# Optimization experiments

Measured on AMD Instinct MI355X. Metric: run time of the kernel, lower is better.

Reference implementation:

```python
import jax, jax.numpy as jnp
import numpy as np

BN_EPS = 1e-5


def setup_inputs() -> dict:
    key = jax.random.key(0)
    ks = jax.random.split(key, 5)
    B, N, M, C = 2, 8192, 8192, 3
    return {
        "x": jax.random.normal(ks[0], (B, N, C), dtype=jnp.float32),
        "y": jax.random.normal(ks[1], (B, M, C), dtype=jnp.float32),
        "W1": jax.random.normal(ks[2], (256, 20), dtype=jnp.float32) * 0.1,
        "gamma1": jnp.ones((256,), jnp.float32),
        "beta1": jnp.zeros((256,), jnp.float32),
        "mean1": jnp.zeros((256,), jnp.float32),
        "var1": jnp.ones((256,), jnp.float32),
        "W2": jax.random.normal(ks[3], (128, 256), dtype=jnp.float32) * 0.1,
        "gamma2": jnp.ones((128,), jnp.float32),
        "beta2": jnp.zeros((128,), jnp.float32),
        "mean2": jnp.zeros((128,), jnp.float32),
        "var2": jnp.ones((128,), jnp.float32),
        "W3": jax.random.normal(ks[4], (1, 128), dtype=jnp.float32) * 0.1,
        "k": 20,
    }


def _bn(x, gamma, beta, mean, var):
    # x: [B, C, N]; inference-mode BatchNorm1d
    inv = gamma * jax.lax.rsqrt(var + BN_EPS)
    return x * inv[None, :, None] + (beta - mean * inv)[None, :, None]


def reference(x, y, W1, gamma1, beta1, mean1, var1,
              W2, gamma2, beta2, mean2, var2, W3, k):
    # x: [B,N,C], y: [B,M,C]
    xx = jnp.sum(x * x, axis=-1)                      # [B,N]
    yy = jnp.sum(y * y, axis=-1)                      # [B,M]
    inner = jnp.einsum('bnc,bmc->bnm', x, y)          # [B,N,M]
    # negative squared pairwise distance (as in torch code)
    pd = 2.0 * inner - xx[:, :, None] - yy[:, None, :]
    dist, _ = jax.lax.top_k(pd, k)                    # [B,N,k], descending = k nearest
    feat = jnp.transpose(dist, (0, 2, 1))             # [B,k,N]
    h = jax.nn.relu(_bn(jnp.einsum('oc,bcn->bon', W1, feat), gamma1, beta1, mean1, var1))
    h = jax.nn.relu(_bn(jnp.einsum('oc,bcn->bon', W2, h), gamma2, beta2, mean2, var2))
    out = jax.nn.sigmoid(jnp.einsum('oc,bcn->bon', W3, h))  # [B,1,N]
    return jnp.transpose(out, (0, 2, 1))              # [B,N,1]
```

## Files before the change

kernel.cpp:

```cpp
#include <hip/hip_runtime.h>
#include <hip/hip_bf16.h>
#include <math.h>


#define M_CAND 8192
#define NROWS 16384
#define KSEL 20
#define MPL 8

__device__ __forceinline__ float med3f(float a, float b, float c) {
    return __builtin_amdgcn_fmed3f(a, b, c);
}

__global__ __launch_bounds__(256) void k_prep_y(const float* __restrict__ y,
                                                float4* __restrict__ ys4) {
    int idx = blockIdx.x * 256 + threadIdx.x;
    float y0 = y[idx * 3 + 0];
    float y1 = y[idx * 3 + 1];
    float y2 = y[idx * 3 + 2];
    ys4[idx] = make_float4(y0, y1, y2, y0 * y0 + y1 * y1 + y2 * y2);
}

__global__ __launch_bounds__(256) void k_transpose_w2(const float* __restrict__ w2,
                                                      float* __restrict__ w2t) {
    int idx = blockIdx.x * 256 + threadIdx.x;
    int o = idx >> 8;
    int k = idx & 255;
    w2t[k * 128 + o] = w2[idx];
}

__global__ __launch_bounds__(256, 4) void k_knn(const float* __restrict__ x,
                                                const float4* __restrict__ ys4,
                                                float* __restrict__ dfeat) {
    __shared__ float sm[4][64 * 21];
    const int wid  = threadIdx.x >> 6;
    const int lane = threadIdx.x & 63;
    const int row  = blockIdx.x * 4 + wid;
    const int b    = row >> 13;
    const float x0 = x[row * 3 + 0];
    const float x1 = x[row * 3 + 1];
    const float x2 = x[row * 3 + 2];
    const float tx0 = 2.0f * x0, tx1 = 2.0f * x1, tx2 = 2.0f * x2;
    const float xxn = -(x0 * x0 + x1 * x1 + x2 * x2);
    const float4* yb = ys4 + b * M_CAND;

    float bl[MPL];
#pragma unroll
    for (int j = 0; j < MPL; ++j) bl[j] = -3.0e38f;

    for (int t = 0; t < M_CAND / 256; ++t) {
        const float4* p = yb + t * 256 + lane;
        float4 cc[4];
        cc[0] = p[0]; cc[1] = p[64]; cc[2] = p[128]; cc[3] = p[192];
#pragma unroll
        for (int j = 0; j < 4; ++j) {
            float v = fmaf(tx0, cc[j].x, fmaf(tx1, cc[j].y, fmaf(tx2, cc[j].z, xxn))) - cc[j].w;
#pragma unroll
            for (int jj = MPL - 1; jj >= 1; --jj) bl[jj] = med3f(v, bl[jj - 1], bl[jj]);
            bl[0] = fmaxf(bl[0], v);
        }
    }

    float* myp = sm[wid] + lane * (MPL + 1);
#pragma unroll
    for (int j = 0; j < MPL; ++j) myp[j] = bl[j];
    myp[MPL] = -3.0e38f;
    asm volatile("s_waitcnt lgkmcnt(0)" ::: "memory");

    int ptr = 0;
    float sel = 0.0f;
    for (int r = 0; r < KSEL; ++r) {
        float head = myp[ptr];
        float mx = head;
#pragma unroll
        for (int off = 32; off >= 1; off >>= 1) mx = fmaxf(mx, __shfl_xor(mx, off, 64));
        unsigned long long ball = __ballot(head == mx);
        int winner = (int)__ffsll(ball) - 1;
        ptr += (lane == winner) ? 1 : 0;
        if (lane == r) sel = mx;
    }

    bool need_exact = (__ballot(ptr >= MPL) != 0ULL);
    if (need_exact) {
        float a[KSEL];
#pragma unroll
        for (int j = 0; j < KSEL; ++j) a[j] = -3.0e38f;
        for (int t = 0; t < M_CAND / 256; ++t) {
            const float4* p = yb + t * 256 + lane;
            float4 cc[4];
            cc[0] = p[0]; cc[1] = p[64]; cc[2] = p[128]; cc[3] = p[192];
#pragma unroll
            for (int j = 0; j < 4; ++j) {
                float v = fmaf(tx0, cc[j].x, fmaf(tx1, cc[j].y, fmaf(tx2, cc[j].z, xxn))) - cc[j].w;
#pragma unroll
                for (int jj = KSEL - 1; jj >= 1; --jj) a[jj] = med3f(v, a[jj - 1], a[jj]);
                a[0] = fmaxf(a[0], v);
            }
        }
        float* mq = sm[wid] + lane * (KSEL + 1);
#pragma unroll
        for (int j = 0; j < KSEL; ++j) mq[j] = a[j];
        mq[KSEL] = -3.0e38f;
        asm volatile("s_waitcnt lgkmcnt(0)" ::: "memory");
        int ptr2 = 0;
        for (int r = 0; r < KSEL; ++r) {
            float head = mq[ptr2];
            float mx = head;
#pragma unroll
            for (int off = 32; off >= 1; off >>= 1) mx = fmaxf(mx, __shfl_xor(mx, off, 64));
            unsigned long long ball = __ballot(head == mx);
            int winner = (int)__ffsll(ball) - 1;
            ptr2 += (lane == winner) ? 1 : 0;
            if (lane == r) sel = mx;
        }
    }

    if (lane < KSEL) dfeat[row * KSEL + lane] = sel;
}

__global__ __launch_bounds__(256) void k_mlp1(const float* __restrict__ dfeat,
                                              const float* __restrict__ W1,
                                              const float* __restrict__ g1,
                                              const float* __restrict__ be1,
                                              const float* __restrict__ mu1,
                                              const float* __restrict__ va1,
                                              float* __restrict__ h1g) {
    const int o = threadIdx.x;
    const int rowbase = blockIdx.x * 64;
    float w[KSEL];
#pragma unroll
    for (int j = 0; j < KSEL; j += 4) {
        float4 q = *(const float4*)(W1 + o * KSEL + j);
        w[j] = q.x; w[j + 1] = q.y; w[j + 2] = q.z; w[j + 3] = q.w;
    }
    const float s  = g1[o] * rsqrtf(va1[o] + 1e-5f);
    const float bc = be1[o] - mu1[o] * s;
    for (int r = 0; r < 64; ++r) {
        const float* dr = dfeat + (size_t)(rowbase + r) * KSEL;
        float dv[KSEL];
#pragma unroll
        for (int j = 0; j < KSEL; j += 4) {
            float4 q = *(const float4*)(dr + j);
            dv[j] = q.x; dv[j + 1] = q.y; dv[j + 2] = q.z; dv[j + 3] = q.w;
        }
        float acc0 = 0.f, acc1 = 0.f;
#pragma unroll
        for (int j = 0; j < KSEL; j += 2) {
            acc0 = fmaf(w[j], dv[j], acc0);
            acc1 = fmaf(w[j + 1], dv[j + 1], acc1);
        }
        float hv = fmaxf(0.f, fmaf(s, acc0 + acc1, bc));
        h1g[(size_t)(rowbase + r) * 256 + o] = hv;
    }
}

__global__ __launch_bounds__(256) void k_mlp2(const float* __restrict__ h1g,
                                              const float* __restrict__ W2T,
                                              const float* __restrict__ g2,
                                              const float* __restrict__ be2,
                                              const float* __restrict__ mu2,
                                              const float* __restrict__ va2,
                                              const float* __restrict__ W3,
                                              float* __restrict__ partial) {
    __shared__ float w2l[256 * 64];
    const int t = threadIdx.x;
    const int ohalf = blockIdx.x & 1;
    const int rowbase = (blockIdx.x >> 1) * 64;
    const int obase = ohalf * 64;

    {
        const int oo4 = (t & 15) * 4;
        const int k0  = t >> 4;
        for (int i = 0; i < 16; ++i) {
            int k = k0 + 16 * i;
            float4 q = *(const float4*)(W2T + k * 128 + obase + oo4);
            *(float4*)(&w2l[k * 64 + oo4]) = q;
        }
    }
    __syncthreads();

    const int og = t & 15;
    const int rq = t >> 4;
    float acc[4][4];
#pragma unroll
    for (int r = 0; r < 4; ++r)
#pragma unroll
        for (int i = 0; i < 4; ++i) acc[r][i] = 0.f;

    const float* hrow = h1g + (size_t)(rowbase + rq * 4) * 256;
    for (int kq = 0; kq < 64; ++kq) {
        const int k = kq * 4;
        float4 hq[4];
        hq[0] = *(const float4*)(hrow + 0 * 256 + k);
        hq[1] = *(const float4*)(hrow + 1 * 256 + k);
        hq[2] = *(const float4*)(hrow + 2 * 256 + k);
        hq[3] = *(const float4*)(hrow + 3 * 256 + k);
        float4 wq[4];
        wq[0] = *(const float4*)(&w2l[(k + 0) * 64 + og * 4]);
        wq[1] = *(const float4*)(&w2l[(k + 1) * 64 + og * 4]);
        wq[2] = *(const float4*)(&w2l[(k + 2) * 64 + og * 4]);
        wq[3] = *(const float4*)(&w2l[(k + 3) * 64 + og * 4]);
#pragma unroll
        for (int r = 0; r < 4; ++r) {
            const float* hh = (const float*)&hq[r];
#pragma unroll
            for (int kk = 0; kk < 4; ++kk) {
                const float* ww = (const float*)&wq[kk];
                const float hval = hh[kk];
#pragma unroll
                for (int i = 0; i < 4; ++i)
                    acc[r][i] = fmaf(hval, ww[i], acc[r][i]);
            }
        }
    }

    float s2v[4], b2v[4], w3v[4];
#pragma unroll
    for (int i = 0; i < 4; ++i) {
        const int o = obase + og * 4 + i;
        const float sv = g2[o] * rsqrtf(va2[o] + 1e-5f);
        s2v[i] = sv;
        b2v[i] = be2[o] - mu2[o] * sv;
        w3v[i] = W3[o];
    }
#pragma unroll
    for (int r = 0; r < 4; ++r) {
        float c = 0.f;
#pragma unroll
        for (int i = 0; i < 4; ++i) {
            float h2 = fmaxf(0.f, fmaf(s2v[i], acc[r][i], b2v[i]));
            c = fmaf(w3v[i], h2, c);
        }
#pragma unroll
        for (int off = 8; off >= 1; off >>= 1) c += __shfl_xor(c, off, 64);
        if (og == 0) partial[ohalf * NROWS + rowbase + rq * 4 + r] = c;
    }
}

__global__ __launch_bounds__(256) void k_out(const float* __restrict__ partial,
                                             float* __restrict__ out) {
    int i = blockIdx.x * 256 + threadIdx.x;
    float z = partial[i] + partial[NROWS + i];
    out[i] = 1.0f / (1.0f + expf(-z));
}

extern "C" void kernel_launch(void* const* d_in, const int* in_sizes, int n_in,
                              void* d_out, int out_size, void* d_ws, size_t ws_size,
                              hipStream_t stream) {
    const float* x   = (const float*)d_in[0];
    const float* y   = (const float*)d_in[1];
    const float* W1  = (const float*)d_in[2];
    const float* g1  = (const float*)d_in[3];
    const float* be1 = (const float*)d_in[4];
    const float* mu1 = (const float*)d_in[5];
    const float* va1 = (const float*)d_in[6];
    const float* W2  = (const float*)d_in[7];
    const float* g2  = (const float*)d_in[8];
    const float* be2 = (const float*)d_in[9];
    const float* mu2 = (const float*)d_in[10];
    const float* va2 = (const float*)d_in[11];
    const float* W3  = (const float*)d_in[12];
    float* out = (float*)d_out;

    char* ws = (char*)d_ws;
    float4* ys4  = (float4*)(ws);
    float* dfeat = (float*)(ws + 262144);
    float* w2t   = (float*)(ws + 262144 + 1310720);
    float* h1    = (float*)(ws + 262144 + 1310720 + 131072);
    float* part  = (float*)(ws + 262144 + 1310720 + 131072 + 16777216);

    k_prep_y      <<<64, 256, 0, stream>>>(y, ys4);
    k_transpose_w2<<<128, 256, 0, stream>>>(W2, w2t);
    k_knn         <<<4096, 256, 0, stream>>>(x, ys4, dfeat);
    k_mlp1        <<<256, 256, 0, stream>>>(dfeat, W1, g1, be1, mu1, va1, h1);
    k_mlp2        <<<512, 256, 0, stream>>>(h1, w2t, g2, be2, mu2, va2, W3, part);
    k_out         <<<64, 256, 0, stream>>>(part, out);
}
```

Baseline: 117.2 us.

## Pack candidate pairs for packed-FMA distance, shrink per-lane list, merge prep kernels

Candidate points are repacked so two candidates share float4 slots, and the distance is computed with packed two-wide FMA. The per-lane top list drops from 8 to 4 entries, which cuts med3 work per candidate, but the exact 20-wide fallback pass will trigger more often. The y-prep and W2-transpose kernels are merged into a single launch. mlp1 now uses more blocks with fewer rows each, giving more parallelism.

```diff
diff --git a/kernel.cpp b/kernel.cpp
--- a/kernel.cpp
+++ b/kernel.cpp
@@ -6,31 +6,46 @@
 #define M_CAND 8192
 #define NROWS 16384
 #define KSEL 20
-#define MPL 8
+#define MPL 4
+
+typedef float v2f __attribute__((ext_vector_type(2)));
 
 __device__ __forceinline__ float med3f(float a, float b, float c) {
     return __builtin_amdgcn_fmed3f(a, b, c);
 }
 
-__global__ __launch_bounds__(256) void k_prep_y(const float* __restrict__ y,
-                                                float4* __restrict__ ys4) {
+__device__ __forceinline__ v2f fma2(v2f a, v2f b, v2f c) {
+#if __has_builtin(__builtin_elementwise_fma)
+    return __builtin_elementwise_fma(a, b, c);
+#else
+    v2f r; r.x = fmaf(a.x, b.x, c.x); r.y = fmaf(a.y, b.y, c.y); return r;
+#endif
+}
+
+__global__ __launch_bounds__(256) void k_prep(const float* __restrict__ y,
+                                              const float* __restrict__ w2,
+                                              float4* __restrict__ ysp,
+                                              float* __restrict__ w2t) {
     int idx = blockIdx.x * 256 + threadIdx.x;
-    float y0 = y[idx * 3 + 0];
-    float y1 = y[idx * 3 + 1];
-    float y2 = y[idx * 3 + 2];
-    ys4[idx] = make_float4(y0, y1, y2, y0 * y0 + y1 * y1 + y2 * y2);
-}
-
-__global__ __launch_bounds__(256) void k_transpose_w2(const float* __restrict__ w2,
-                                                      float* __restrict__ w2t) {
-    int idx = blockIdx.x * 256 + threadIdx.x;
-    int o = idx >> 8;
-    int k = idx & 255;
-    w2t[k * 128 + o] = w2[idx];
+    if (idx < 8192) {
+        int b = idx >> 12, q = idx & 4095;
+        const float* p0 = y + (size_t)(b * M_CAND + 2 * q) * 3;
+        float a0 = p0[0], a1 = p0[1], a2 = p0[2];
+        float b0 = p0[3], b1 = p0[4], b2 = p0[5];
+        float nwa = -(a0 * a0 + a1 * a1 + a2 * a2);
+        float nwb = -(b0 * b0 + b1 * b1 + b2 * b2);
+        float4* base = ysp + b * 8192;
+        base[q]        = make_float4(a0, b0, a1, b1);
+        base[4096 + q] = make_float4(a2, b2, nwa, nwb);
+    } else {
+        int j = idx - 8192;
+        int o = j >> 8, kk = j & 255;
+        w2t[kk * 128 + o] = w2[j];
+    }
 }
 
 __global__ __launch_bounds__(256, 4) void k_knn(const float* __restrict__ x,
-                                                const float4* __restrict__ ys4,
+                                                const float4* __restrict__ ysp,
                                                 float* __restrict__ dfeat) {
     __shared__ float sm[4][64 * 21];
     const int wid  = threadIdx.x >> 6;
@@ -40,24 +55,38 @@
     const float x0 = x[row * 3 + 0];
     const float x1 = x[row * 3 + 1];
     const float x2 = x[row * 3 + 2];
-    const float tx0 = 2.0f * x0, tx1 = 2.0f * x1, tx2 = 2.0f * x2;
+    const v2f tx0p = {2.0f * x0, 2.0f * x0};
+    const v2f tx1p = {2.0f * x1, 2.0f * x1};
+    const v2f tx2p = {2.0f * x2, 2.0f * x2};
     const float xxn = -(x0 * x0 + x1 * x1 + x2 * x2);
-    const float4* yb = ys4 + b * M_CAND;
+    const v2f xxnp = {xxn, xxn};
+    const float4* yb = ysp + b * 8192;
 
     float bl[MPL];
 #pragma unroll
     for (int j = 0; j < MPL; ++j) bl[j] = -3.0e38f;
 
-    for (int t = 0; t < M_CAND / 256; ++t) {
-        const float4* p = yb + t * 256 + lane;
-        float4 cc[4];
-        cc[0] = p[0]; cc[1] = p[64]; cc[2] = p[128]; cc[3] = p[192];
-#pragma unroll
-        for (int j = 0; j < 4; ++j) {
-            float v = fmaf(tx0, cc[j].x, fmaf(tx1, cc[j].y, fmaf(tx2, cc[j].z, xxn))) - cc[j].w;
-#pragma unroll
-            for (int jj = MPL - 1; jj >= 1; --jj) bl[jj] = med3f(v, bl[jj - 1], bl[jj]);
-            bl[0] = fmaxf(bl[0], v);
+#pragma unroll 2
+    for (int t = 0; t < 16; ++t) {
+        const float4* pa = yb + t * 256 + lane;
+        const float4* pb = pa + 4096;
+        float4 A[4], Bv[4];
+        A[0]  = pa[0];  A[1]  = pa[64];  A[2]  = pa[128];  A[3]  = pa[192];
+        Bv[0] = pb[0];  Bv[1] = pb[64];  Bv[2] = pb[128];  Bv[3] = pb[192];
+#pragma unroll
+        for (int i = 0; i < 4; ++i) {
+            v2f y0p = {A[i].x,  A[i].y};
+            v2f y1p = {A[i].z,  A[i].w};
+            v2f y2p = {Bv[i].x, Bv[i].y};
+            v2f nwp = {Bv[i].z, Bv[i].w};
+            v2f pd = fma2(tx0p, y0p, fma2(tx1p, y1p, fma2(tx2p, y2p, xxnp))) + nwp;
+            float va = pd.x, vb = pd.y;
+#pragma unroll
+            for (int jj = MPL - 1; jj >= 1; --jj) bl[jj] = med3f(va, bl[jj - 1], bl[jj]);
+            bl[0] = fmaxf(bl[0], va);
+#pragma unroll
+            for (int jj = MPL - 1; jj >= 1; --jj) bl[jj] = med3f(vb, bl[jj - 1], bl[jj]);
+            bl[0] = fmaxf(bl[0], vb);
         }
     }
 
@@ -85,16 +114,26 @@
         float a[KSEL];
 #pragma unroll
         for (int j = 0; j < KSEL; ++j) a[j] = -3.0e38f;
-        for (int t = 0; t < M_CAND / 256; ++t) {
-            const float4* p = yb + t * 256 + lane;
-            float4 cc[4];
-            cc[0] = p[0]; cc[1] = p[64]; cc[2] = p[128]; cc[3] = p[192];
-#pragma unroll
-            for (int j = 0; j < 4; ++j) {
-                float v = fmaf(tx0, cc[j].x, fmaf(tx1, cc[j].y, fmaf(tx2, cc[j].z, xxn))) - cc[j].w;
-#pragma unroll
-                for (int jj = KSEL - 1; jj >= 1; --jj) a[jj] = med3f(v, a[jj - 1], a[jj]);
-                a[0] = fmaxf(a[0], v);
+        for (int t = 0; t < 16; ++t) {
+            const float4* pa = yb + t * 256 + lane;
+            const float4* pb = pa + 4096;
+            float4 A[4], Bv[4];
+            A[0]  = pa[0];  A[1]  = pa[64];  A[2]  = pa[128];  A[3]  = pa[192];
+            Bv[0] = pb[0];  Bv[1] = pb[64];  Bv[2] = pb[128];  Bv[3] = pb[192];
+#pragma unroll
+            for (int i = 0; i < 4; ++i) {
+                v2f y0p = {A[i].x,  A[i].y};
+                v2f y1p = {A[i].z,  A[i].w};
+                v2f y2p = {Bv[i].x, Bv[i].y};
+                v2f nwp = {Bv[i].z, Bv[i].w};
+                v2f pd = fma2(tx0p, y0p, fma2(tx1p, y1p, fma2(tx2p, y2p, xxnp))) + nwp;
+                float va = pd.x, vb = pd.y;
+#pragma unroll
+                for (int jj = KSEL - 1; jj >= 1; --jj) a[jj] = med3f(va, a[jj - 1], a[jj]);
+                a[0] = fmaxf(a[0], va);
+#pragma unroll
+                for (int jj = KSEL - 1; jj >= 1; --jj) a[jj] = med3f(vb, a[jj - 1], a[jj]);
+                a[0] = fmaxf(a[0], vb);
             }
         }
         float* mq = sm[wid] + lane * (KSEL + 1);
@@ -126,7 +165,7 @@
                                               const float* __restrict__ va1,
                                               float* __restrict__ h1g) {
     const int o = threadIdx.x;
-    const int rowbase = blockIdx.x * 64;
+    const int rowbase = blockIdx.x * 16;
     float w[KSEL];
 #pragma unroll
     for (int j = 0; j < KSEL; j += 4) {
@@ -135,7 +174,8 @@
     }
     const float s  = g1[o] * rsqrtf(va1[o] + 1e-5f);
     const float bc = be1[o] - mu1[o] * s;
-    for (int r = 0; r < 64; ++r) {
+#pragma unroll 4
+    for (int r = 0; r < 16; ++r) {
         const float* dr = dfeat + (size_t)(rowbase + r) * KSEL;
         float dv[KSEL];
 #pragma unroll
@@ -263,16 +303,15 @@
     float* out = (float*)d_out;
 
     char* ws = (char*)d_ws;
-    float4* ys4  = (float4*)(ws);
+    float4* ysp  = (float4*)(ws);
     float* dfeat = (float*)(ws + 262144);
     float* w2t   = (float*)(ws + 262144 + 1310720);
     float* h1    = (float*)(ws + 262144 + 1310720 + 131072);
     float* part  = (float*)(ws + 262144 + 1310720 + 131072 + 16777216);
 
-    k_prep_y      <<<64, 256, 0, stream>>>(y, ys4);
-    k_transpose_w2<<<128, 256, 0, stream>>>(W2, w2t);
-    k_knn         <<<4096, 256, 0, stream>>>(x, ys4, dfeat);
-    k_mlp1        <<<256, 256, 0, stream>>>(dfeat, W1, g1, be1, mu1, va1, h1);
-    k_mlp2        <<<512, 256, 0, stream>>>(h1, w2t, g2, be2, mu2, va2, W3, part);
-    k_out         <<<64, 256, 0, stream>>>(part, out);
-}
+    k_prep <<<160, 256, 0, stream>>>(y, W2, ysp, w2t);
+    k_knn  <<<4096, 256, 0, stream>>>(x, ysp, dfeat);
+    k_mlp1 <<<1024, 256, 0, stream>>>(dfeat, W1, g1, be1, mu1, va1, h1);
+    k_mlp2 <<<512, 256, 0, stream>>>(h1, w2t, g2, be2, mu2, va2, W3, part);
+    k_out  <<<64, 256, 0, stream>>>(part, out);
+}
```

Result: slower. 126.3 us (+7.8%).

## Fuse MLP stages, merge prep kernels, shrink per-lane kNN list, SoA candidate layout

Applied to the files above, without the earlier changes.

Merges the y-prep and W2-transpose kernels into one launch. It fuses MLP layer 1, layer 2, the W3 reduction and the sigmoid into a single kernel that keeps h1 in shared memory, so the 16 MB h1 round trip through global memory and two launches go away. The kNN candidates move to a structure-of-arrays layout with the squared norm pre-negated, and the next tile is software-prefetched. The per-lane partial top-k list shrinks from 8 to 4 entries, which cuts med3 work but makes the exact fallback pass more likely to run.

```diff
diff --git a/kernel.cpp b/kernel.cpp
--- a/kernel.cpp
+++ b/kernel.cpp
@@ -6,31 +6,35 @@
 #define M_CAND 8192
 #define NROWS 16384
 #define KSEL 20
-#define MPL 8
+#define MPL 4
 
 __device__ __forceinline__ float med3f(float a, float b, float c) {
     return __builtin_amdgcn_fmed3f(a, b, c);
 }
 
-__global__ __launch_bounds__(256) void k_prep_y(const float* __restrict__ y,
-                                                float4* __restrict__ ys4) {
+__global__ __launch_bounds__(256) void k_prep(const float* __restrict__ y,
+                                              const float* __restrict__ w2,
+                                              float* __restrict__ ys,
+                                              float* __restrict__ w2t) {
     int idx = blockIdx.x * 256 + threadIdx.x;
-    float y0 = y[idx * 3 + 0];
-    float y1 = y[idx * 3 + 1];
-    float y2 = y[idx * 3 + 2];
-    ys4[idx] = make_float4(y0, y1, y2, y0 * y0 + y1 * y1 + y2 * y2);
-}
-
-__global__ __launch_bounds__(256) void k_transpose_w2(const float* __restrict__ w2,
-                                                      float* __restrict__ w2t) {
-    int idx = blockIdx.x * 256 + threadIdx.x;
-    int o = idx >> 8;
-    int k = idx & 255;
-    w2t[k * 128 + o] = w2[idx];
+    if (idx < NROWS) {
+        int b = idx >> 13, m = idx & 8191;
+        const float* p = y + (size_t)idx * 3;
+        float y0 = p[0], y1 = p[1], y2 = p[2];
+        float* base = ys + (size_t)b * 4 * M_CAND + m;
+        base[0]          = y0;
+        base[M_CAND]     = y1;
+        base[2 * M_CAND] = y2;
+        base[3 * M_CAND] = -(y0 * y0 + y1 * y1 + y2 * y2);
+    } else {
+        int j = idx - NROWS;
+        int o = j >> 8, kk = j & 255;
+        w2t[kk * 128 + o] = w2[j];
+    }
 }
 
 __global__ __launch_bounds__(256, 4) void k_knn(const float* __restrict__ x,
-                                                const float4* __restrict__ ys4,
+                                                const float* __restrict__ ys,
                                                 float* __restrict__ dfeat) {
     __shared__ float sm[4][64 * 21];
     const int wid  = threadIdx.x >> 6;
@@ -42,23 +46,33 @@
     const float x2 = x[row * 3 + 2];
     const float tx0 = 2.0f * x0, tx1 = 2.0f * x1, tx2 = 2.0f * x2;
     const float xxn = -(x0 * x0 + x1 * x1 + x2 * x2);
-    const float4* yb = ys4 + b * M_CAND;
+    const float4* q0 = (const float4*)(ys + (size_t)(b * 4 + 0) * M_CAND) + lane;
+    const float4* q1 = (const float4*)(ys + (size_t)(b * 4 + 1) * M_CAND) + lane;
+    const float4* q2 = (const float4*)(ys + (size_t)(b * 4 + 2) * M_CAND) + lane;
+    const float4* q3 = (const float4*)(ys + (size_t)(b * 4 + 3) * M_CAND) + lane;
 
     float bl[MPL];
 #pragma unroll
     for (int j = 0; j < MPL; ++j) bl[j] = -3.0e38f;
 
-    for (int t = 0; t < M_CAND / 256; ++t) {
-        const float4* p = yb + t * 256 + lane;
-        float4 cc[4];
-        cc[0] = p[0]; cc[1] = p[64]; cc[2] = p[128]; cc[3] = p[192];
+    float4 c0 = q0[0], c1 = q1[0], c2 = q2[0], c3 = q3[0];
+#pragma unroll 1
+    for (int t = 0; t < 32; ++t) {
+        const int nt = ((t + 1) & 31) * 64;
+        float4 n0 = q0[nt], n1 = q1[nt], n2 = q2[nt], n3 = q3[nt];
+        const float* e0 = (const float*)&c0;
+        const float* e1 = (const float*)&c1;
+        const float* e2 = (const float*)&c2;
+        const float* e3 = (const float*)&c3;
 #pragma unroll
         for (int j = 0; j < 4; ++j) {
-            float v = fmaf(tx0, cc[j].x, fmaf(tx1, cc[j].y, fmaf(tx2, cc[j].z, xxn))) - cc[j].w;
-#pragma unroll
-            for (int jj = MPL - 1; jj >= 1; --jj) bl[jj] = med3f(v, bl[jj - 1], bl[jj]);
+            float v = fmaf(tx0, e0[j], fmaf(tx1, e1[j], fmaf(tx2, e2[j], xxn))) + e3[j];
+            bl[3] = med3f(v, bl[2], bl[3]);
+            bl[2] = med3f(v, bl[1], bl[2]);
+            bl[1] = med3f(v, bl[0], bl[1]);
             bl[0] = fmaxf(bl[0], v);
         }
+        c0 = n0; c1 = n1; c2 = n2; c3 = n3;
     }
 
     float* myp = sm[wid] + lane * (MPL + 1);
@@ -85,13 +99,15 @@
         float a[KSEL];
 #pragma unroll
         for (int j = 0; j < KSEL; ++j) a[j] = -3.0e38f;
-        for (int t = 0; t < M_CAND / 256; ++t) {
-            const float4* p = yb + t * 256 + lane;
-            float4 cc[4];
-            cc[0] = p[0]; cc[1] = p[64]; cc[2] = p[128]; cc[3] = p[192];
+        for (int t = 0; t < 32; ++t) {
+            float4 d0 = q0[t * 64], d1 = q1[t * 64], d2 = q2[t * 64], d3 = q3[t * 64];
+            const float* e0 = (const float*)&d0;
+            const float* e1 = (const float*)&d1;
+            const float* e2 = (const float*)&d2;
+            const float* e3 = (const float*)&d3;
 #pragma unroll
             for (int j = 0; j < 4; ++j) {
-                float v = fmaf(tx0, cc[j].x, fmaf(tx1, cc[j].y, fmaf(tx2, cc[j].z, xxn))) - cc[j].w;
+                float v = fmaf(tx0, e0[j], fmaf(tx1, e1[j], fmaf(tx2, e2[j], xxn))) + e3[j];
 #pragma unroll
                 for (int jj = KSEL - 1; jj >= 1; --jj) a[jj] = med3f(v, a[jj - 1], a[jj]);
                 a[0] = fmaxf(a[0], v);
@@ -118,130 +134,135 @@
     if (lane < KSEL) dfeat[row * KSEL + lane] = sel;
 }
 
-__global__ __launch_bounds__(256) void k_mlp1(const float* __restrict__ dfeat,
-                                              const float* __restrict__ W1,
-                                              const float* __restrict__ g1,
-                                              const float* __restrict__ be1,
-                                              const float* __restrict__ mu1,
-                                              const float* __restrict__ va1,
-                                              float* __restrict__ h1g) {
-    const int o = threadIdx.x;
-    const int rowbase = blockIdx.x * 64;
-    float w[KSEL];
-#pragma unroll
-    for (int j = 0; j < KSEL; j += 4) {
-        float4 q = *(const float4*)(W1 + o * KSEL + j);
-        w[j] = q.x; w[j + 1] = q.y; w[j + 2] = q.z; w[j + 3] = q.w;
-    }
-    const float s  = g1[o] * rsqrtf(va1[o] + 1e-5f);
-    const float bc = be1[o] - mu1[o] * s;
-    for (int r = 0; r < 64; ++r) {
-        const float* dr = dfeat + (size_t)(rowbase + r) * KSEL;
-        float dv[KSEL];
-#pragma unroll
-        for (int j = 0; j < KSEL; j += 4) {
-            float4 q = *(const float4*)(dr + j);
-            dv[j] = q.x; dv[j + 1] = q.y; dv[j + 2] = q.z; dv[j + 3] = q.w;
-        }
-        float acc0 = 0.f, acc1 = 0.f;
-#pragma unroll
-        for (int j = 0; j < KSEL; j += 2) {
-            acc0 = fmaf(w[j], dv[j], acc0);
-            acc1 = fmaf(w[j + 1], dv[j + 1], acc1);
-        }
-        float hv = fmaxf(0.f, fmaf(s, acc0 + acc1, bc));
-        h1g[(size_t)(rowbase + r) * 256 + o] = hv;
-    }
-}
-
-__global__ __launch_bounds__(256) void k_mlp2(const float* __restrict__ h1g,
-                                              const float* __restrict__ W2T,
-                                              const float* __restrict__ g2,
-                                              const float* __restrict__ be2,
-                                              const float* __restrict__ mu2,
-                                              const float* __restrict__ va2,
-                                              const float* __restrict__ W3,
-                                              float* __restrict__ partial) {
+__global__ __launch_bounds__(256) void k_mlp(const float* __restrict__ dfeat,
+                                             const float* __restrict__ W1,
+                                             const float* __restrict__ g1,
+                                             const float* __restrict__ be1,
+                                             const float* __restrict__ mu1,
+                                             const float* __restrict__ va1,
+                                             const float* __restrict__ W2T,
+                                             const float* __restrict__ g2,
+                                             const float* __restrict__ be2,
+                                             const float* __restrict__ mu2,
+                                             const float* __restrict__ va2,
+                                             const float* __restrict__ W3,
+                                             float* __restrict__ out) {
+    __shared__ float h1l[32 * 260];
     __shared__ float w2l[256 * 64];
+    __shared__ float featl[640];
     const int t = threadIdx.x;
-    const int ohalf = blockIdx.x & 1;
-    const int rowbase = (blockIdx.x >> 1) * 64;
-    const int obase = ohalf * 64;
-
+    const int rowbase = blockIdx.x * 32;
+
+    for (int i = t; i < 160; i += 256)
+        ((float4*)featl)[i] = *(const float4*)(dfeat + (size_t)rowbase * KSEL + i * 4);
     {
         const int oo4 = (t & 15) * 4;
         const int k0  = t >> 4;
         for (int i = 0; i < 16; ++i) {
             int k = k0 + 16 * i;
-            float4 q = *(const float4*)(W2T + k * 128 + obase + oo4);
-            *(float4*)(&w2l[k * 64 + oo4]) = q;
-        }
+            *(float4*)(&w2l[k * 64 + oo4]) = *(const float4*)(W2T + k * 128 + oo4);
+        }
+    }
+
+    float w[KSEL];
+#pragma unroll
+    for (int j = 0; j < KSEL; j += 4) {
+        float4 q = *(const float4*)(W1 + t * KSEL + j);
+        w[j] = q.x; w[j + 1] = q.y; w[j + 2] = q.z; w[j + 3] = q.w;
+    }
+    const float s1  = g1[t] * rsqrtf(va1[t] + 1e-5f);
+    const float bc1 = be1[t] - mu1[t] * s1;
+
+    __syncthreads();
+
+    for (int r = 0; r < 32; ++r) {
+        const float* fr = featl + r * KSEL;
+        float acc0 = 0.f, acc1 = 0.f;
+#pragma unroll
+        for (int j = 0; j < KSEL; j += 2) {
+            acc0 = fmaf(w[j], fr[j], acc0);
+            acc1 = fmaf(w[j + 1], fr[j + 1], acc1);
+        }
+        h1l[r * 260 + t] = fmaxf(0.f, fmaf(s1, acc0 + acc1, bc1));
     }
     __syncthreads();
 
     const int og = t & 15;
     const int rq = t >> 4;
-    float acc[4][4];
-#pragma unroll
-    for (int r = 0; r < 4; ++r)
-#pragma unroll
-        for (int i = 0; i < 4; ++i) acc[r][i] = 0.f;
-
-    const float* hrow = h1g + (size_t)(rowbase + rq * 4) * 256;
-    for (int kq = 0; kq < 64; ++kq) {
-        const int k = kq * 4;
-        float4 hq[4];
-        hq[0] = *(const float4*)(hrow + 0 * 256 + k);
-        hq[1] = *(const float4*)(hrow + 1 * 256 + k);
-        hq[2] = *(const float4*)(hrow + 2 * 256 + k);
-        hq[3] = *(const float4*)(hrow + 3 * 256 + k);
-        float4 wq[4];
-        wq[0] = *(const float4*)(&w2l[(k + 0) * 64 + og * 4]);
-        wq[1] = *(const float4*)(&w2l[(k + 1) * 64 + og * 4]);
-        wq[2] = *(const float4*)(&w2l[(k + 2) * 64 + og * 4]);
-        wq[3] = *(const float4*)(&w2l[(k + 3) * 64 + og * 4]);
-#pragma unroll
-        for (int r = 0; r < 4; ++r) {
-            const float* hh = (const float*)&hq[r];
-#pragma unroll
-            for (int kk = 0; kk < 4; ++kk) {
-                const float* ww = (const float*)&wq[kk];
-                const float hval = hh[kk];
-#pragma unroll
-                for (int i = 0; i < 4; ++i)
-                    acc[r][i] = fmaf(hval, ww[i], acc[r][i]);
-            }
-        }
-    }
-
-    float s2v[4], b2v[4], w3v[4];
-#pragma unroll
-    for (int i = 0; i < 4; ++i) {
-        const int o = obase + og * 4 + i;
-        const float sv = g2[o] * rsqrtf(va2[o] + 1e-5f);
-        s2v[i] = sv;
-        b2v[i] = be2[o] - mu2[o] * sv;
-        w3v[i] = W3[o];
-    }
-#pragma unroll
-    for (int r = 0; r < 4; ++r) {
-        float c = 0.f;
+    float cacc[2] = {0.f, 0.f};
+
+    for (int half = 0; half < 2; ++half) {
+        if (half == 1) {
+            __syncthreads();
+            const int oo4 = (t & 15) * 4;
+            const int k0  = t >> 4;
+            for (int i = 0; i < 16; ++i) {
+                int k = k0 + 16 * i;
+                *(float4*)(&w2l[k * 64 + oo4]) = *(const float4*)(W2T + k * 128 + 64 + oo4);
+            }
+            __syncthreads();
+        }
+
+        float acc[2][4];
+#pragma unroll
+        for (int r = 0; r < 2; ++r)
+#pragma unroll
+            for (int i = 0; i < 4; ++i) acc[r][i] = 0.f;
+
+        for (int kq = 0; kq < 64; ++kq) {
+            const int k = kq * 4;
+            float4 hq[2];
+#pragma unroll
+            for (int rr = 0; rr < 2; ++rr)
+                hq[rr] = *(const float4*)(&h1l[(rq * 2 + rr) * 260 + k]);
+            float4 wq[4];
+#pragma unroll
+            for (int kk = 0; kk < 4; ++kk)
+                wq[kk] = *(const float4*)(&w2l[(k + kk) * 64 + og * 4]);
+#pragma unroll
+            for (int r = 0; r < 2; ++r) {
+                const float* hh = (const float*)&hq[r];
+#pragma unroll
+                for (int kk = 0; kk < 4; ++kk) {
+                    const float* ww = (const float*)&wq[kk];
+                    const float hval = hh[kk];
+#pragma unroll
+                    for (int i = 0; i < 4; ++i)
+                        acc[r][i] = fmaf(hval, ww[i], acc[r][i]);
+                }
+            }
+        }
+
+        float s2v[4], b2v[4], w3v[4];
 #pragma unroll
         for (int i = 0; i < 4; ++i) {
-            float h2 = fmaxf(0.f, fmaf(s2v[i], acc[r][i], b2v[i]));
-            c = fmaf(w3v[i], h2, c);
-        }
-#pragma unroll
-        for (int off = 8; off >= 1; off >>= 1) c += __shfl_xor(c, off, 64);
-        if (og == 0) partial[ohalf * NROWS + rowbase + rq * 4 + r] = c;
-    }
-}
-
-__global__ __launch_bounds__(256) void k_out(const float* __restrict__ partial,
-                                             float* __restrict__ out) {
-    int i = blockIdx.x * 256 + threadIdx.x;
-    float z = partial[i] + partial[NROWS + i];
-    out[i] = 1.0f / (1.0f + expf(-z));
+            const int o = half * 64 + og * 4 + i;
+            const float sv = g2[o] * rsqrtf(va2[o] + 1e-5f);
+            s2v[i] = sv;
+            b2v[i] = be2[o] - mu2[o] * sv;
+            w3v[i] = W3[o];
+        }
+#pragma unroll
+        for (int r = 0; r < 2; ++r) {
+            float c = 0.f;
+#pragma unroll
+            for (int i = 0; i < 4; ++i) {
+                float h2 = fmaxf(0.f, fmaf(s2v[i], acc[r][i], b2v[i]));
+                c = fmaf(w3v[i], h2, c);
+            }
+#pragma unroll
+            for (int off = 8; off >= 1; off >>= 1) c += __shfl_xor(c, off, 64);
+            cacc[r] += c;
+        }
+    }
+
+    if (og == 0) {
+#pragma unroll
+        for (int r = 0; r < 2; ++r) {
+            float z = cacc[r];
+            out[rowbase + rq * 2 + r] = 1.0f / (1.0f + expf(-z));
+        }
+    }
 }
 
 extern "C" void kernel_launch(void* const* d_in, const int* in_sizes, int n_in,
@@ -263,16 +284,12 @@
     float* out = (float*)d_out;
 
     char* ws = (char*)d_ws;
-    float4* ys4  = (float4*)(ws);
+    float* ys    = (float*)(ws);
     float* dfeat = (float*)(ws + 262144);
     float* w2t   = (float*)(ws + 262144 + 1310720);
-    float* h1    = (float*)(ws + 262144 + 1310720 + 131072);
-    float* part  = (float*)(ws + 262144 + 1310720 + 131072 + 16777216);
-
-    k_prep_y      <<<64, 256, 0, stream>>>(y, ys4);
-    k_transpose_w2<<<128, 256, 0, stream>>>(W2, w2t);
-    k_knn         <<<4096, 256, 0, stream>>>(x, ys4, dfeat);
-    k_mlp1        <<<256, 256, 0, stream>>>(dfeat, W1, g1, be1, mu1, va1, h1);
-    k_mlp2        <<<512, 256, 0, stream>>>(h1, w2t, g2, be2, mu2, va2, W3, part);
-    k_out         <<<64, 256, 0, stream>>>(part, out);
-}
+
+    k_prep<<<192, 256, 0, stream>>>(y, W2, ys, w2t);
+    k_knn <<<4096, 256, 0, stream>>>(x, ys, dfeat);
+    k_mlp <<<512, 256, 0, stream>>>(dfeat, W1, g1, be1, mu1, va1,
+                                    w2t, g2, be2, mu2, va2, W3, out);
+}
```

Measured after the change: 127.6 us. 1.09x slower.
